# Kernel tuning notes

Measured on AMD Instinct MI355X. Metric: run time of the kernel, lower is better.

The kernel has to match this reference:

```python
import jax, jax.numpy as jnp
import numpy as np

B, S, D, H, DK, DV = 2, 2048, 1024, 16, 64, 64


def setup_inputs() -> dict:
    key = jax.random.key(0)
    ks = jax.random.split(key, 12)
    inp = {
        "query": jax.random.normal(ks[0], (B, S, D), jnp.float32),
        "key":   jax.random.normal(ks[1], (B, S, D), jnp.float32),
        "value": jax.random.normal(ks[2], (B, S, D), jnp.float32),
        # additive mask broadcast over per-head [B,S,S] scores (zeros = no masking)
        "mask":  jnp.zeros((S, S), jnp.float32),
        # stacked per-head projection params (math-equivalent to H separate Linears)
        "Wq": jax.random.normal(ks[3], (H, D, DK), jnp.float32) / np.sqrt(D),
        "bq": jax.random.normal(ks[4], (H, DK), jnp.float32) * 0.02,
        "Wk": jax.random.normal(ks[5], (H, D, DK), jnp.float32) / np.sqrt(D),
        "bk": jax.random.normal(ks[6], (H, DK), jnp.float32) * 0.02,
        "Wv": jax.random.normal(ks[7], (H, D, DV), jnp.float32) / np.sqrt(D),
        "bv": jax.random.normal(ks[8], (H, DV), jnp.float32) * 0.02,
        "Wo": jax.random.normal(ks[9], (H * DV, D), jnp.float32) / np.sqrt(H * DV),
        "bo": jax.random.normal(ks[10], (D,), jnp.float32) * 0.02,
    }
    return inp


def reference(query, key, value, mask, Wq, bq, Wk, bk, Wv, bv, Wo, bo):
    # per-head projections, vectorized over heads
    q = jnp.einsum("bsd,hdk->bhsk", query, Wq) + bq[None, :, None, :]
    k = jnp.einsum("bsd,hdk->bhsk", key, Wk) + bk[None, :, None, :]
    v = jnp.einsum("bsd,hdv->bhsv", value, Wv) + bv[None, :, None, :]
    # explicit QK^T softmax V, scale by sqrt(dim_k) (key.size(-1))
    scores = jnp.einsum("bhsk,bhtk->bhst", q, k) / jnp.sqrt(jnp.asarray(DK, q.dtype))
    scores = scores + mask  # broadcast [S,S] -> [B,H,S,S]
    attn = jax.nn.softmax(scores, axis=-1)
    out = jnp.einsum("bhst,bhtv->bhsv", attn, v)
    # concat heads along last dim: [B,S,H*DV]
    out = out.transpose(0, 2, 1, 3).reshape(B, S, H * DV)
    return out @ Wo + bo
```

## Files before the change

kernel.cpp:

```cpp
#include <hip/hip_runtime.h>
#include <stdint.h>

typedef __bf16 bf16;
typedef float f32x4 __attribute__((ext_vector_type(4)));
typedef __bf16 bf16x8 __attribute__((ext_vector_type(8)));
typedef __bf16 bf16x4 __attribute__((ext_vector_type(4)));

__device__ __forceinline__ void async_load16(const void* g, void* l) {
    __builtin_amdgcn_global_load_lds(
        (const __attribute__((address_space(1))) void*)g,
        (__attribute__((address_space(3))) void*)l, 16, 0, 0);
}

__global__ void detect_dtype(const unsigned short* __restrict__ q, int* __restrict__ flag) {
    __shared__ int cnt;
    if (threadIdx.x == 0) cnt = 0;
    __syncthreads();
    int c = 0;
    for (int i = threadIdx.x; i < 4096; i += 256) {
        int e = (q[i] >> 7) & 0xFF;
        if (e >= 0xC0) ++c;
    }
    atomicAdd(&cnt, c);
    __syncthreads();
    if (threadIdx.x == 0) { flag[0] = (cnt > 64) ? 1 : 0; flag[1] = 0; }
}

__global__ void prep(const void* __restrict__ qv, const void* __restrict__ vv,
                     const void* __restrict__ wq, const void* __restrict__ wk,
                     const void* __restrict__ wv, const void* __restrict__ wo,
                     const unsigned int* __restrict__ mask,
                     bf16* __restrict__ Xq, bf16* __restrict__ Xv,
                     bf16* __restrict__ WqT, bf16* __restrict__ WoT,
                     int* __restrict__ flag) {
    __shared__ bf16 t[32][33];
    const int f    = flag[0];
    const int task = blockIdx.z;
    const int bid  = blockIdx.x + 64 * blockIdx.y;

    if (task < 2) {
        const void* x = task ? vv : qv;
        bf16* o = task ? Xv : Xq;
        size_t i = ((size_t)bid * 256 + threadIdx.x) * 8;
        if (f) {
            f32x4 a = ((const f32x4*)x)[i / 4];
            f32x4 b = ((const f32x4*)x)[i / 4 + 1];
            bf16x8 v;
            for (int j = 0; j < 4; ++j) { v[j] = (bf16)a[j]; v[4 + j] = (bf16)b[j]; }
            *(bf16x8*)(o + i) = v;
        } else {
            *(bf16x8*)(o + i) = *(const bf16x8*)((const bf16*)x + i);
        }
    } else if (task < 5) {
        if (bid >= 1024) return;
        const void* in = (task == 2) ? wq : ((task == 3) ? wk : wv);
        int sub = bid >> 6, rem = bid & 63;
        int c0 = (rem & 1) * 32, r0 = (rem >> 1) * 32;
        int tx = threadIdx.x & 31, ty = threadIdx.x >> 5;
        size_t base = (size_t)sub * 65536;
        if (f) {
            const float* inF = (const float*)in;
            for (int i = 0; i < 32; i += 8)
                t[ty + i][tx] = (bf16)inF[base + (size_t)(r0 + ty + i) * 64 + (c0 + tx)];
        } else {
            const bf16* inB = (const bf16*)in;
            for (int i = 0; i < 32; i += 8)
                t[ty + i][tx] = inB[base + (size_t)(r0 + ty + i) * 64 + (c0 + tx)];
        }
        __syncthreads();
        bf16* o = WqT + ((size_t)(task - 2) * 16 + sub) * 65536;
        for (int i = 0; i < 32; i += 8)
            o[(size_t)(c0 + ty + i) * 1024 + (r0 + tx)] = t[tx][ty + i];
    } else if (task == 5) {
        if (bid >= 1024) return;
        int c0 = (bid & 31) * 32, r0 = (bid >> 5) * 32;
        int tx = threadIdx.x & 31, ty = threadIdx.x >> 5;
        if (f) {
            const float* inF = (const float*)wo;
            for (int i = 0; i < 32; i += 8)
                t[ty + i][tx] = (bf16)inF[(size_t)(r0 + ty + i) * 1024 + (c0 + tx)];
        } else {
            const bf16* inB = (const bf16*)wo;
            for (int i = 0; i < 32; i += 8)
                t[ty + i][tx] = inB[(size_t)(r0 + ty + i) * 1024 + (c0 + tx)];
        }
        __syncthreads();
        for (int i = 0; i < 32; i += 8)
            WoT[(size_t)(c0 + ty + i) * 1024 + (r0 + tx)] = t[tx][ty + i];
    } else {
        const long nvec = (f ? 4194304L : 2097152L) / 4;
        unsigned int acc = 0;
        long stride = 2048L * 256;
        for (long i = (long)bid * 256 + threadIdx.x; i < nvec; i += stride) {
            uint4 v = ((const uint4*)mask)[i];
            acc |= v.x | v.y | v.z | v.w;
        }
        if (acc) atomicOr(flag + 1, 1);
    }
}

__global__ __launch_bounds__(256, 3) void gemm_qkv(
    const bf16* __restrict__ Xq, const void* __restrict__ keyRaw,
    const bf16* __restrict__ Xv, const bf16* __restrict__ Bt,
    const void* __restrict__ b0, const void* __restrict__ b1, const void* __restrict__ b2,
    bf16* __restrict__ Qp, bf16* __restrict__ Kp, bf16* __restrict__ Vt,
    const int* __restrict__ flag) {
    __shared__ __attribute__((aligned(16))) unsigned char AsRaw[128 * 64 * 4];
    __shared__ __attribute__((aligned(16))) bf16 Bs[128 * 64];

    const int f = flag[0];
    const int K = 1024, N = 1024;
    const int z = blockIdx.z;
    const int af = (z == 1) ? f : 0;
    const void* Av   = (z == 0) ? (const void*)Xq : ((z == 1) ? keyRaw : (const void*)Xv);
    const void* bias = (z == 0) ? b0 : ((z == 1) ? b1 : b2);
    const bf16* B    = Bt + (size_t)z * 1024 * 1024;

    const int tid  = threadIdx.x;
    const int lane = tid & 63;
    const int w    = tid >> 6;
    const int quad = lane >> 4;
    const int mrow = lane & 15;
    const int m0 = blockIdx.y * 128;
    const int n0 = blockIdx.x * 128;
    const int wm = (w & 1) * 64;
    const int wn = (w >> 1) * 64;

    f32x4 acc[4][4] = {};

    for (int k0 = 0; k0 < K; k0 += 64) {
        if (af) {
            for (int it = 0; it < 8; ++it) {
                int ci  = it * 256 + tid;
                int row = ci >> 4, pc = ci & 15;
                int swz = ((row & 7) << 1) | ((row >> 3) & 1);
                int gc  = pc ^ swz;
                async_load16((const float*)Av + (size_t)(m0 + row) * K + k0 + gc * 4,
                             AsRaw + (size_t)(it * 256 + w * 64) * 16);
            }
        } else {
            for (int it = 0; it < 4; ++it) {
                int ci  = it * 256 + tid;
                int row = ci >> 3, pc = ci & 7;
                int gc  = pc ^ (row & 7);
                async_load16((const bf16*)Av + (size_t)(m0 + row) * K + k0 + gc * 8,
                             (bf16*)AsRaw + (size_t)(it * 256 + w * 64) * 8);
            }
        }
        for (int it = 0; it < 4; ++it) {
            int ci  = it * 256 + tid;
            int row = ci >> 3, pc = ci & 7;
            int gc  = pc ^ (row & 7);
            async_load16(B + (size_t)(n0 + row) * K + k0 + gc * 8,
                         Bs + (size_t)(it * 256 + w * 64) * 8);
        }
        __syncthreads();
        for (int kk = 0; kk < 2; ++kk) {
            bf16x8 afr[4], bfr[4];
            if (af) {
                const float* Asf = (const float*)AsRaw;
                for (int mi = 0; mi < 4; ++mi) {
                    int row = wm + mi * 16 + mrow;
                    int swz = ((row & 7) << 1) | ((row >> 3) & 1);
                    int lc  = (kk * 4 + quad) * 2;
                    f32x4 u0 = *(const f32x4*)(Asf + row * 64 + (lc ^ swz) * 4);
                    f32x4 u1 = *(const f32x4*)(Asf + row * 64 + ((lc + 1) ^ swz) * 4);
                    for (int j = 0; j < 4; ++j) {
                        afr[mi][j]     = (bf16)u0[j];
                        afr[mi][4 + j] = (bf16)u1[j];
                    }
                }
            } else {
                const bf16* Asb = (const bf16*)AsRaw;
                for (int mi = 0; mi < 4; ++mi) {
                    int row = wm + mi * 16 + mrow;
                    int pc  = (kk * 4 + quad) ^ (row & 7);
                    afr[mi] = *(const bf16x8*)(Asb + row * 64 + pc * 8);
                }
            }
            for (int ni = 0; ni < 4; ++ni) {
                int row = wn + ni * 16 + mrow;
                int pc  = (kk * 4 + quad) ^ (row & 7);
                bfr[ni] = *(const bf16x8*)(Bs + row * 64 + pc * 8);
            }
            for (int mi = 0; mi < 4; ++mi)
                for (int ni = 0; ni < 4; ++ni)
                    acc[mi][ni] = __builtin_amdgcn_mfma_f32_16x16x32_bf16(
                        afr[mi], bfr[ni], acc[mi][ni], 0, 0, 0);
        }
        __syncthreads();
    }

    const float scl = (z == 0) ? 0.18033688f : 1.0f;
    for (int ni = 0; ni < 4; ++ni) {
        int n    = n0 + wn + ni * 16 + mrow;
        float bv = f ? ((const float*)bias)[n] : (float)((const bf16*)bias)[n];
        for (int mi = 0; mi < 4; ++mi) {
            int mb = m0 + wm + mi * 16 + quad * 4;
            if (z == 2) {
                bf16x4 pk;
                for (int r = 0; r < 4; ++r) pk[r] = (bf16)(acc[mi][ni][r] + bv);
                *(bf16x4*)(Vt + (((size_t)(mb >> 11) * 1024 + n) << 11) + (mb & 2047)) = pk;
            } else {
                bf16* P = (z == 0) ? Qp : Kp;
                for (int r = 0; r < 4; ++r)
                    P[(size_t)(mb + r) * N + n] = (bf16)((acc[mi][ni][r] + bv) * scl);
            }
        }
    }
}

__global__ __launch_bounds__(256, 2) void gemm_out(
    const bf16* __restrict__ A, const bf16* __restrict__ Bt,
    const void* __restrict__ bias, void* __restrict__ Cout,
    const int* __restrict__ flag) {
    __shared__ __attribute__((aligned(16))) bf16 As[128 * 64];
    __shared__ __attribute__((aligned(16))) bf16 Bs[64 * 64];

    const int f = flag[0];
    const int K = 1024, N = 1024;
    const int tid  = threadIdx.x;
    const int lane = tid & 63;
    const int w    = tid >> 6;
    const int quad = lane >> 4;
    const int mrow = lane & 15;
    const int m0 = blockIdx.y * 128;
    const int n0 = blockIdx.x * 64;
    const int wm = (w & 1) * 64;
    const int wn = (w >> 1) * 32;

    f32x4 acc[4][2] = {};

    for (int k0 = 0; k0 < K; k0 += 64) {
        for (int it = 0; it < 4; ++it) {
            int ci  = it * 256 + tid;
            int row = ci >> 3, pc = ci & 7;
            int gc  = pc ^ (row & 7);
            async_load16(A + (size_t)(m0 + row) * K + k0 + gc * 8,
                         As + (size_t)(it * 256 + w * 64) * 8);
        }
        for (int it = 0; it < 2; ++it) {
            int ci  = it * 256 + tid;
            int row = ci >> 3, pc = ci & 7;
            int gc  = pc ^ (row & 7);
            async_load16(Bt + (size_t)(n0 + row) * K + k0 + gc * 8,
                         Bs + (size_t)(it * 256 + w * 64) * 8);
        }
        __syncthreads();
        for (int kk = 0; kk < 2; ++kk) {
            bf16x8 afr[4], bfr[2];
            for (int mi = 0; mi < 4; ++mi) {
                int row = wm + mi * 16 + mrow;
                int pc  = (kk * 4 + quad) ^ (row & 7);
                afr[mi] = *(const bf16x8*)(As + row * 64 + pc * 8);
            }
            for (int ni = 0; ni < 2; ++ni) {
                int row = wn + ni * 16 + mrow;
                int pc  = (kk * 4 + quad) ^ (row & 7);
                bfr[ni] = *(const bf16x8*)(Bs + row * 64 + pc * 8);
            }
            for (int mi = 0; mi < 4; ++mi)
                for (int ni = 0; ni < 2; ++ni)
                    acc[mi][ni] = __builtin_amdgcn_mfma_f32_16x16x32_bf16(
                        afr[mi], bfr[ni], acc[mi][ni], 0, 0, 0);
        }
        __syncthreads();
    }

    for (int ni = 0; ni < 2; ++ni) {
        int n    = n0 + wn + ni * 16 + mrow;
        float bv = f ? ((const float*)bias)[n] : (float)((const bf16*)bias)[n];
        for (int mi = 0; mi < 4; ++mi) {
            int mb = m0 + wm + mi * 16 + quad * 4;
            for (int r = 0; r < 4; ++r) {
                float val = acc[mi][ni][r] + bv;
                if (f) ((float*)Cout)[(size_t)(mb + r) * N + n] = val;
                else   ((bf16*)Cout)[(size_t)(mb + r) * N + n] = (bf16)val;
            }
        }
    }
}

__global__ __launch_bounds__(256, 2) void flash_attn(
    const bf16* __restrict__ Qp, const bf16* __restrict__ Kp,
    const bf16* __restrict__ Vt, const void* __restrict__ maskv,
    bf16* __restrict__ O, const int* __restrict__ flag) {
    __shared__ __attribute__((aligned(16))) bf16 Ks[2][4096];
    __shared__ __attribute__((aligned(16))) bf16 Vs[2][4096];
    __shared__ __attribute__((aligned(16))) bf16 Ps[128 * 72];

    const int f       = flag[0];
    const int useMask = flag[1];
    const int tid  = threadIdx.x;
    const int lane = tid & 63;
    const int w    = tid >> 6;
    const int quad = lane >> 4;
    const int c    = lane & 15;
    const int s0   = blockIdx.x * 128;
    const int h    = blockIdx.y;
    const int b    = blockIdx.z;

    const size_t qkBase = (size_t)b * 2048 * 1024 + h * 64;
    const size_t vtBase = ((size_t)b * 1024 + h * 64) * 2048;

    const int ci0 = tid, ci1 = 256 + tid;
    const int r0 = ci0 >> 3, g0 = (ci0 & 7) ^ (r0 & 7);
    const int r1 = ci1 >> 3, g1 = (ci1 & 7) ^ (r1 & 7);
    const bf16* kp0 = Kp + qkBase + (size_t)r0 * 1024 + g0 * 8;
    const bf16* kp1 = Kp + qkBase + (size_t)r1 * 1024 + g1 * 8;
    const bf16* vp0 = Vt + vtBase + (size_t)r0 * 2048 + g0 * 8;
    const bf16* vp1 = Vt + vtBase + (size_t)r1 * 2048 + g1 * 8;

#define STAGE(B_, T_) do {                                                             \
        async_load16(kp0 + (size_t)(T_) * 1024, &Ks[B_][(size_t)(w * 64) * 8]);        \
        async_load16(kp1 + (size_t)(T_) * 1024, &Ks[B_][(size_t)(256 + w * 64) * 8]);  \
        async_load16(vp0 + (T_),                &Vs[B_][(size_t)(w * 64) * 8]);        \
        async_load16(vp1 + (T_),                &Vs[B_][(size_t)(256 + w * 64) * 8]);  \
    } while (0)

    const bf16* kf0 = &Ks[0][c * 64 + ((0 + quad) ^ (c & 7)) * 8];
    const bf16* kf1 = &Ks[0][c * 64 + ((4 + quad) ^ (c & 7)) * 8];
    const bf16* vf0 = &Vs[0][c * 64 + ((0 + quad) ^ (c & 7)) * 8];
    const bf16* vf1 = &Vs[0][c * 64 + ((4 + quad) ^ (c & 7)) * 8];
    bf16*       pw0 = Ps + (w * 32 + c) * 72 + quad * 4;
    bf16*       pw1 = Ps + (w * 32 + 16 + c) * 72 + quad * 4;
    const bf16* pr0 = Ps + (w * 32 + c) * 72 + quad * 8;
    const bf16* pr1 = Ps + (w * 32 + 16 + c) * 72 + quad * 8;

    bf16x8 aq[2][2];
    for (int hh = 0; hh < 2; ++hh) {
        const bf16* qrow = Qp + qkBase + (size_t)(s0 + w * 32 + hh * 16 + c) * 1024;
        aq[hh][0] = *(const bf16x8*)(qrow + quad * 8);
        aq[hh][1] = *(const bf16x8*)(qrow + 32 + quad * 8);
    }

    f32x4 o_acc[2][4] = {};
    float l_s[2] = {0.f, 0.f};

    const size_t mb0 = (size_t)(s0 + w * 32 + c) * 2048;
    const size_t mb1 = (size_t)(s0 + w * 32 + 16 + c) * 2048;

#define FCOMP(IB_, T_) do {                                                              \
        f32x4 sc[2][4] = {};                                                             \
        _Pragma("unroll") for (int tt = 0; tt < 4; ++tt) {                               \
            bf16x8 ak0 = *(const bf16x8*)(kf0 + (IB_) * 4096 + tt * 1024);               \
            bf16x8 ak1 = *(const bf16x8*)(kf1 + (IB_) * 4096 + tt * 1024);               \
            sc[0][tt] = __builtin_amdgcn_mfma_f32_16x16x32_bf16(ak0, aq[0][0], sc[0][tt], 0, 0, 0); \
            sc[0][tt] = __builtin_amdgcn_mfma_f32_16x16x32_bf16(ak1, aq[0][1], sc[0][tt], 0, 0, 0); \
            sc[1][tt] = __builtin_amdgcn_mfma_f32_16x16x32_bf16(ak0, aq[1][0], sc[1][tt], 0, 0, 0); \
            sc[1][tt] = __builtin_amdgcn_mfma_f32_16x16x32_bf16(ak1, aq[1][1], sc[1][tt], 0, 0, 0); \
        }                                                                                \
        if (useMask) {                                                                   \
            _Pragma("unroll") for (int hh = 0; hh < 2; ++hh) {                           \
                const size_t mr = (hh ? mb1 : mb0) + (T_);                               \
                _Pragma("unroll") for (int tt = 0; tt < 4; ++tt) {                       \
                    if (f) {                                                             \
                        f32x4 mk = *(const f32x4*)((const float*)maskv + mr + tt * 16 + quad * 4); \
                        for (int r = 0; r < 4; ++r) sc[hh][tt][r] += mk[r] * 1.44269504f; \
                    } else {                                                             \
                        bf16x4 mk = *(const bf16x4*)((const bf16*)maskv + mr + tt * 16 + quad * 4); \
                        for (int r = 0; r < 4; ++r) sc[hh][tt][r] += (float)mk[r] * 1.44269504f; \
                    }                                                                    \
                }                                                                        \
            }                                                                            \
        }                                                                                \
        _Pragma("unroll") for (int hh = 0; hh < 2; ++hh) {                               \
            float rsum = 0.f;                                                            \
            bf16* pw = hh ? pw1 : pw0;                                                   \
            _Pragma("unroll") for (int tt = 0; tt < 4; ++tt) {                           \
                bf16x4 pk;                                                               \
                for (int r = 0; r < 4; ++r) {                                            \
                    float p = exp2f(sc[hh][tt][r]);                                      \
                    rsum += p;                                                           \
                    pk[r] = (bf16)p;                                                     \
                }                                                                        \
                *(bf16x4*)(pw + tt * 16) = pk;                                           \
            }                                                                            \
            l_s[hh] += rsum;                                                             \
        }                                                                                \
        _Pragma("unroll") for (int kk = 0; kk < 2; ++kk) {                               \
            bf16x8 ap0 = *(const bf16x8*)((kk ? pr0 + 32 : pr0));                        \
            bf16x8 ap1 = *(const bf16x8*)((kk ? pr1 + 32 : pr1));                        \
            const bf16* vfb = kk ? vf1 : vf0;                                            \
            _Pragma("unroll") for (int ni = 0; ni < 4; ++ni) {                           \
                bf16x8 bv = *(const bf16x8*)(vfb + (IB_) * 4096 + ni * 1024);            \
                o_acc[0][ni] = __builtin_amdgcn_mfma_f32_16x16x32_bf16(ap0, bv, o_acc[0][ni], 0, 0, 0); \
                o_acc[1][ni] = __builtin_amdgcn_mfma_f32_16x16x32_bf16(ap1, bv, o_acc[1][ni], 0, 0, 0); \
            }                                                                            \
        }                                                                                \
    } while (0)

    STAGE(0, 0);
    for (int t0 = 0; t0 < 2048; t0 += 128) {
        __syncthreads();
        STAGE(1, t0 + 64);
        FCOMP(0, t0);
        __syncthreads();
        if (t0 + 128 < 2048) STAGE(0, t0 + 128);
        FCOMP(1, t0 + 64);
    }
#undef STAGE
#undef FCOMP

    for (int hh = 0; hh < 2; ++hh) {
        float ls = l_s[hh];
        ls += __shfl_xor(ls, 16, 64);
        ls += __shfl_xor(ls, 32, 64);
        for (int r = 0; r < 4; ++r) {
            float lv   = __shfl(ls, quad * 4 + r, 64);
            float inv  = 1.0f / lv;
            size_t roff = (size_t)(b * 2048 + s0 + w * 32 + hh * 16 + quad * 4 + r) * 1024 + h * 64;
            for (int ni = 0; ni < 4; ++ni)
                O[roff + ni * 16 + c] = (bf16)(o_acc[hh][ni][r] * inv);
        }
    }
}

extern "C" void kernel_launch(void* const* d_in, const int* in_sizes, int n_in,
                              void* d_out, int out_size, void* d_ws, size_t ws_size,
                              hipStream_t stream) {
    bf16* ws = (bf16*)d_ws;
    (void)in_sizes; (void)n_in; (void)out_size; (void)ws_size;

    const size_t MM = 1024 * 1024;
    int*  flag = (int*)ws;
    bf16* WqT  = ws + 8;
    bf16* WoT  = WqT + 3 * MM;
    bf16* Qp   = WoT + MM;
    bf16* Kp   = Qp + 4 * MM;
    bf16* Xq   = Kp + 4 * MM;
    bf16* AO   = Xq;
    bf16* Xv   = (bf16*)d_out;
    bf16* Vt   = (bf16*)d_out + 4 * MM;

    detect_dtype<<<1, 256, 0, stream>>>((const unsigned short*)d_in[0], flag);

    prep<<<dim3(64, 32, 7), 256, 0, stream>>>(d_in[0], d_in[2], d_in[4], d_in[6],
                                              d_in[8], d_in[10],
                                              (const unsigned int*)d_in[3],
                                              Xq, Xv, WqT, WoT, flag);

    gemm_qkv<<<dim3(8, 32, 3), 256, 0, stream>>>(Xq, d_in[1], Xv, WqT,
                                                 d_in[5], d_in[7], d_in[9],
                                                 Qp, Kp, Vt, flag);

    flash_attn<<<dim3(16, 16, 2), 256, 0, stream>>>(Qp, Kp, Vt, d_in[3], AO, flag);

    gemm_out<<<dim3(16, 32, 1), 256, 0, stream>>>(AO, WoT, d_in[11], d_out, flag);
}
```

Measured before the change: 268.8 us.

## Pre-convert key input to bf16 and shrink projection GEMM N-tile to 64

```diff
diff --git a/kernel.cpp b/kernel.cpp
--- a/kernel.cpp
+++ b/kernel.cpp
@@ -27,10 +27,11 @@
 }
 
 __global__ void prep(const void* __restrict__ qv, const void* __restrict__ vv,
+                     const void* __restrict__ kv,
                      const void* __restrict__ wq, const void* __restrict__ wk,
                      const void* __restrict__ wv, const void* __restrict__ wo,
                      const unsigned int* __restrict__ mask,
-                     bf16* __restrict__ Xq, bf16* __restrict__ Xv,
+                     bf16* __restrict__ Xq, bf16* __restrict__ Xv, bf16* __restrict__ Xk,
                      bf16* __restrict__ WqT, bf16* __restrict__ WoT,
                      int* __restrict__ flag) {
     __shared__ bf16 t[32][33];
@@ -38,9 +39,9 @@
     const int task = blockIdx.z;
     const int bid  = blockIdx.x + 64 * blockIdx.y;
 
-    if (task < 2) {
-        const void* x = task ? vv : qv;
-        bf16* o = task ? Xv : Xq;
+    if (task < 3) {
+        const void* x = (task == 0) ? qv : ((task == 1) ? vv : kv);
+        bf16* o = (task == 0) ? Xq : ((task == 1) ? Xv : Xk);
         size_t i = ((size_t)bid * 256 + threadIdx.x) * 8;
         if (f) {
             f32x4 a = ((const f32x4*)x)[i / 4];
@@ -51,9 +52,9 @@
         } else {
             *(bf16x8*)(o + i) = *(const bf16x8*)((const bf16*)x + i);
         }
-    } else if (task < 5) {
+    } else if (task < 6) {
         if (bid >= 1024) return;
-        const void* in = (task == 2) ? wq : ((task == 3) ? wk : wv);
+        const void* in = (task == 3) ? wq : ((task == 4) ? wk : wv);
         int sub = bid >> 6, rem = bid & 63;
         int c0 = (rem & 1) * 32, r0 = (rem >> 1) * 32;
         int tx = threadIdx.x & 31, ty = threadIdx.x >> 5;
@@ -68,10 +69,10 @@
                 t[ty + i][tx] = inB[base + (size_t)(r0 + ty + i) * 64 + (c0 + tx)];
         }
         __syncthreads();
-        bf16* o = WqT + ((size_t)(task - 2) * 16 + sub) * 65536;
+        bf16* o = WqT + ((size_t)(task - 3) * 16 + sub) * 65536;
         for (int i = 0; i < 32; i += 8)
             o[(size_t)(c0 + ty + i) * 1024 + (r0 + tx)] = t[tx][ty + i];
-    } else if (task == 5) {
+    } else if (task == 6) {
         if (bid >= 1024) return;
         int c0 = (bid & 31) * 32, r0 = (bid >> 5) * 32;
         int tx = threadIdx.x & 31, ty = threadIdx.x >> 5;
@@ -99,20 +100,19 @@
     }
 }
 
-__global__ __launch_bounds__(256, 3) void gemm_qkv(
-    const bf16* __restrict__ Xq, const void* __restrict__ keyRaw,
-    const bf16* __restrict__ Xv, const bf16* __restrict__ Bt,
+__global__ __launch_bounds__(256, 4) void gemm_proj(
+    const bf16* __restrict__ Xq, const bf16* __restrict__ Xk, const bf16* __restrict__ Xv,
+    const bf16* __restrict__ Bt,
     const void* __restrict__ b0, const void* __restrict__ b1, const void* __restrict__ b2,
     bf16* __restrict__ Qp, bf16* __restrict__ Kp, bf16* __restrict__ Vt,
-    const int* __restrict__ flag) {
-    __shared__ __attribute__((aligned(16))) unsigned char AsRaw[128 * 64 * 4];
-    __shared__ __attribute__((aligned(16))) bf16 Bs[128 * 64];
+    const int* __restrict__ flag, int zbase) {
+    __shared__ __attribute__((aligned(16))) bf16 As[128 * 64];
+    __shared__ __attribute__((aligned(16))) bf16 Bs[64 * 64];
 
     const int f = flag[0];
     const int K = 1024, N = 1024;
-    const int z = blockIdx.z;
-    const int af = (z == 1) ? f : 0;
-    const void* Av   = (z == 0) ? (const void*)Xq : ((z == 1) ? keyRaw : (const void*)Xv);
+    const int z = zbase + blockIdx.z;
+    const bf16* A    = (z == 0) ? Xq : ((z == 1) ? Xk : Xv);
     const void* bias = (z == 0) ? b0 : ((z == 1) ? b1 : b2);
     const bf16* B    = Bt + (size_t)z * 1024 * 1024;
 
@@ -122,32 +122,21 @@
     const int quad = lane >> 4;
     const int mrow = lane & 15;
     const int m0 = blockIdx.y * 128;
-    const int n0 = blockIdx.x * 128;
+    const int n0 = blockIdx.x * 64;
     const int wm = (w & 1) * 64;
-    const int wn = (w >> 1) * 64;
-
-    f32x4 acc[4][4] = {};
+    const int wn = (w >> 1) * 32;
+
+    f32x4 acc[4][2] = {};
 
     for (int k0 = 0; k0 < K; k0 += 64) {
-        if (af) {
-            for (int it = 0; it < 8; ++it) {
-                int ci  = it * 256 + tid;
-                int row = ci >> 4, pc = ci & 15;
-                int swz = ((row & 7) << 1) | ((row >> 3) & 1);
-                int gc  = pc ^ swz;
-                async_load16((const float*)Av + (size_t)(m0 + row) * K + k0 + gc * 4,
-                             AsRaw + (size_t)(it * 256 + w * 64) * 16);
-            }
-        } else {
-            for (int it = 0; it < 4; ++it) {
-                int ci  = it * 256 + tid;
-                int row = ci >> 3, pc = ci & 7;
-                int gc  = pc ^ (row & 7);
-                async_load16((const bf16*)Av + (size_t)(m0 + row) * K + k0 + gc * 8,
-                             (bf16*)AsRaw + (size_t)(it * 256 + w * 64) * 8);
-            }
-        }
         for (int it = 0; it < 4; ++it) {
+            int ci  = it * 256 + tid;
+            int row = ci >> 3, pc = ci & 7;
+            int gc  = pc ^ (row & 7);
+            async_load16(A + (size_t)(m0 + row) * K + k0 + gc * 8,
+                         As + (size_t)(it * 256 + w * 64) * 8);
+        }
+        for (int it = 0; it < 2; ++it) {
             int ci  = it * 256 + tid;
             int row = ci >> 3, pc = ci & 7;
             int gc  = pc ^ (row & 7);
@@ -156,43 +145,27 @@
         }
         __syncthreads();
         for (int kk = 0; kk < 2; ++kk) {
-            bf16x8 afr[4], bfr[4];
-            if (af) {
-                const float* Asf = (const float*)AsRaw;
-                for (int mi = 0; mi < 4; ++mi) {
-                    int row = wm + mi * 16 + mrow;
-                    int swz = ((row & 7) << 1) | ((row >> 3) & 1);
-                    int lc  = (kk * 4 + quad) * 2;
-                    f32x4 u0 = *(const f32x4*)(Asf + row * 64 + (lc ^ swz) * 4);
-                    f32x4 u1 = *(const f32x4*)(Asf + row * 64 + ((lc + 1) ^ swz) * 4);
-                    for (int j = 0; j < 4; ++j) {
-                        afr[mi][j]     = (bf16)u0[j];
-                        afr[mi][4 + j] = (bf16)u1[j];
-                    }
-                }
-            } else {
-                const bf16* Asb = (const bf16*)AsRaw;
-                for (int mi = 0; mi < 4; ++mi) {
-                    int row = wm + mi * 16 + mrow;
-                    int pc  = (kk * 4 + quad) ^ (row & 7);
-                    afr[mi] = *(const bf16x8*)(Asb + row * 64 + pc * 8);
-                }
-            }
-            for (int ni = 0; ni < 4; ++ni) {
+            bf16x8 afr[4], bfr[2];
+            for (int mi = 0; mi < 4; ++mi) {
+                int row = wm + mi * 16 + mrow;
+                int pc  = (kk * 4 + quad) ^ (row & 7);
+                afr[mi] = *(const bf16x8*)(As + row * 64 + pc * 8);
+            }
+            for (int ni = 0; ni < 2; ++ni) {
                 int row = wn + ni * 16 + mrow;
                 int pc  = (kk * 4 + quad) ^ (row & 7);
                 bfr[ni] = *(const bf16x8*)(Bs + row * 64 + pc * 8);
             }
             for (int mi = 0; mi < 4; ++mi)
-                for (int ni = 0; ni < 4; ++ni)
+                for (int ni = 0; ni < 2; ++ni)
                     acc[mi][ni] = __builtin_amdgcn_mfma_f32_16x16x32_bf16(
                         afr[mi], bfr[ni], acc[mi][ni], 0, 0, 0);
         }
         __syncthreads();
     }
 
-    const float scl = (z == 0) ? 0.18033688f : 1.0f;
-    for (int ni = 0; ni < 4; ++ni) {
+    const float scl = 0.18033688f;
+    for (int ni = 0; ni < 2; ++ni) {
         int n    = n0 + wn + ni * 16 + mrow;
         float bv = f ? ((const float*)bias)[n] : (float)((const bf16*)bias)[n];
         for (int mi = 0; mi < 4; ++mi) {
@@ -201,10 +174,12 @@
                 bf16x4 pk;
                 for (int r = 0; r < 4; ++r) pk[r] = (bf16)(acc[mi][ni][r] + bv);
                 *(bf16x4*)(Vt + (((size_t)(mb >> 11) * 1024 + n) << 11) + (mb & 2047)) = pk;
+            } else if (z == 1) {
+                for (int r = 0; r < 4; ++r)
+                    Kp[(size_t)(mb + r) * N + n] = (bf16)(acc[mi][ni][r] + bv);
             } else {
-                bf16* P = (z == 0) ? Qp : Kp;
                 for (int r = 0; r < 4; ++r)
-                    P[(size_t)(mb + r) * N + n] = (bf16)((acc[mi][ni][r] + bv) * scl);
+                    Qp[(size_t)(mb + r) * N + n] = (bf16)((acc[mi][ni][r] + bv) * scl);
             }
         }
     }
@@ -370,7 +345,7 @@
             _Pragma("unroll") for (int tt = 0; tt < 4; ++tt) {                           \
                 bf16x4 pk;                                                               \
                 for (int r = 0; r < 4; ++r) {                                            \
-                    float p = exp2f(sc[hh][tt][r]);                                      \
+                    float p = __builtin_amdgcn_exp2f(sc[hh][tt][r]);                     \
                     rsum += p;                                                           \
                     pk[r] = (bf16)p;                                                     \
                 }                                                                        \
@@ -427,6 +402,7 @@
     bf16* WqT  = ws + 8;
     bf16* WoT  = WqT + 3 * MM;
     bf16* Qp   = WoT + MM;
+    bf16* Xk   = Qp;
     bf16* Kp   = Qp + 4 * MM;
     bf16* Xq   = Kp + 4 * MM;
     bf16* AO   = Xq;
@@ -435,14 +411,17 @@
 
     detect_dtype<<<1, 256, 0, stream>>>((const unsigned short*)d_in[0], flag);
 
-    prep<<<dim3(64, 32, 7), 256, 0, stream>>>(d_in[0], d_in[2], d_in[4], d_in[6],
-                                              d_in[8], d_in[10],
+    prep<<<dim3(64, 32, 8), 256, 0, stream>>>(d_in[0], d_in[2], d_in[1],
+                                              d_in[4], d_in[6], d_in[8], d_in[10],
                                               (const unsigned int*)d_in[3],
-                                              Xq, Xv, WqT, WoT, flag);
-
-    gemm_qkv<<<dim3(8, 32, 3), 256, 0, stream>>>(Xq, d_in[1], Xv, WqT,
-                                                 d_in[5], d_in[7], d_in[9],
-                                                 Qp, Kp, Vt, flag);
+                                              Xq, Xv, Xk, WqT, WoT, flag);
+
+    gemm_proj<<<dim3(16, 32, 2), 256, 0, stream>>>(Xq, Xk, Xv, WqT,
+                                                   d_in[5], d_in[7], d_in[9],
+                                                   Qp, Kp, Vt, flag, 1);
+    gemm_proj<<<dim3(16, 32, 1), 256, 0, stream>>>(Xq, Xk, Xv, WqT,
+                                                   d_in[5], d_in[7], d_in[9],
+                                                   Qp, Kp, Vt, flag, 0);
 
     flash_attn<<<dim3(16, 16, 2), 256, 0, stream>>>(Qp, Kp, Vt, d_in[3], AO, flag);
 
```

After: 269.2 us. No clear change (+0.1%).
